# Kernel optimization log

Measured on AMD Instinct MI355X. Metric: run time of the kernel, lower is better.

## Reference

```python
import jax, jax.numpy as jnp
import numpy as np

NUM_HEADS = 8
ATTN_BALANCE = 0.5
EPS = 1e-4  # eps in normalize()


def mp_linear(x, w, gain):
    # MP_Conv with kernel=(1,1): per-output-channel RMS weight renorm then scale.
    # normalize(w): w / (eps + ||w_row|| / sqrt(fan_in)); then * gain / sqrt(fan_in)
    fan_in = w.shape[1]
    n = jnp.linalg.norm(w.astype(jnp.float32), axis=1, keepdims=True)  # (out,1)
    wn = w / (EPS + n / np.sqrt(fan_in))
    wn = wn * (gain / np.sqrt(fan_in))
    return x @ wn.T


def setup_inputs() -> dict:
    key = jax.random.key(0)
    ks = jax.random.split(key, 6)
    B, S, E = 8, 1024, 1024
    H = NUM_HEADS
    return {
        "query": jax.random.normal(ks[0], (B, S, E), jnp.float32),
        "gain_s": jnp.ones((), jnp.float32),
        "gain_t": jnp.ones((), jnp.float32),
        "q_w": jax.random.normal(ks[1], (E, E), jnp.float32),
        "k_w": jax.random.normal(ks[2], (E, E), jnp.float32),
        "v_w": jax.random.normal(ks[3], (E, E), jnp.float32),
        "o_w": jax.random.normal(ks[4], (E, E), jnp.float32),
        "rel_pos_bias": 0.01 * jax.random.normal(ks[5], (H, S, S), jnp.float32),
    }


def reference(query, gain_s, gain_t, q_w, k_w, v_w, o_w, rel_pos_bias):
    # time_dim=0 so the time-dependent branches are inactive; gain_t unused.
    B, S, E = query.shape
    H = NUM_HEADS
    hd = E // H
    # MP projections (1x1 conv == per-position linear), split heads -> (B,H,S,hd)
    q = mp_linear(query, q_w, gain_s).reshape(B, S, H, hd).transpose(0, 2, 1, 3)
    k = mp_linear(query, k_w, gain_s).reshape(B, S, H, hd).transpose(0, 2, 1, 3)
    v = mp_linear(query, v_w, gain_s).reshape(B, S, H, hd).transpose(0, 2, 1, 3)
    # (B,H,S,S) scores, scaled, plus learned relative position bias (seq_len == seq_ln)
    scores = jnp.einsum("bhsd,bhtd->bhst", q, k) / np.sqrt(hd) + rel_pos_bias[None]
    attn = jax.nn.softmax(scores, axis=-1)
    o = jnp.einsum("bhst,bhtd->bhsd", attn, v)
    o = o.transpose(0, 2, 1, 3).reshape(B, S, E)
    out = mp_linear(o, o_w, gain_s)
    # mp_sum residual: lerp(res, out, t) / sqrt((1-t)^2 + t^2)
    t = ATTN_BALANCE
    return (query * (1.0 - t) + out * t) / np.sqrt((1.0 - t) ** 2 + t ** 2)
```

## Files before the change

kernel.cpp:

```cpp
#include <hip/hip_runtime.h>
#include <hip/hip_bf16.h>
#include <math.h>


typedef __attribute__((ext_vector_type(4))) float f32x4;
typedef __attribute__((ext_vector_type(4))) short s16x4;
typedef __attribute__((ext_vector_type(8))) short s16x8;

__device__ __forceinline__ short f2bf(float f) {
  union { __hip_bfloat16 h; short s; } u;
  u.h = __float2bfloat16(f);
  return u.s;
}
__device__ __forceinline__ f32x4 mfma16(s16x8 a, s16x8 b, f32x4 c) {
  return __builtin_amdgcn_mfma_f32_16x16x32_bf16(a, b, c, 0, 0, 0);
}

typedef __attribute__((address_space(1))) const unsigned int* as1_u32p;
typedef __attribute__((address_space(3))) unsigned int* as3_u32p;
__device__ __forceinline__ void g2l16(const short* g, short* l) {
  __builtin_amdgcn_global_load_lds((as1_u32p)g, (as3_u32p)l, 16, 0, 0);
}

__global__ __launch_bounds__(256) void k_wnorm(const float* __restrict__ qw, const float* __restrict__ kw,
                                               const float* __restrict__ vw, const float* __restrict__ ow,
                                               const float* __restrict__ gain, short* __restrict__ wn) {
  const int r = blockIdx.x;
  const int mat = r >> 10;
  const float* W = mat == 0 ? qw : mat == 1 ? kw : mat == 2 ? vw : ow;
  const float* src = W + (size_t)(r & 1023) * 1024;
  const int tid = threadIdx.x;
  f32x4 v = *(const f32x4*)&src[tid * 4];
  float s = v[0]*v[0] + v[1]*v[1] + v[2]*v[2] + v[3]*v[3];
  __shared__ float red[256];
  red[tid] = s; __syncthreads();
  for (int off = 128; off > 0; off >>= 1) {
    if (tid < off) red[tid] += red[tid + off];
    __syncthreads();
  }
  const float scale = gain[0] / (0.0032f + sqrtf(red[0]));
  s16x4 o;
  o[0] = f2bf(v[0]*scale); o[1] = f2bf(v[1]*scale);
  o[2] = f2bf(v[2]*scale); o[3] = f2bf(v[3]*scale);
  *(s16x4*)&wn[(size_t)r * 1024 + tid * 4] = o;
}

__global__ __launch_bounds__(256) void k_cvt(const float* __restrict__ in, short* __restrict__ out, int n4) {
  int idx = blockIdx.x * 256 + threadIdx.x;
  int stride = gridDim.x * 256;
  for (int i = idx; i < n4; i += stride) {
    f32x4 v = ((const f32x4*)in)[i];
    s16x4 o;
    o[0] = f2bf(v[0]); o[1] = f2bf(v[1]); o[2] = f2bf(v[2]); o[3] = f2bf(v[3]);
    ((s16x4*)out)[i] = o;
  }
}

__global__ __launch_bounds__(256) void k_scaleb(const float* __restrict__ in, float* __restrict__ out, int n4) {
  const float L2E = 1.4426950408889634f;
  int idx = blockIdx.x * 256 + threadIdx.x;
  int stride = gridDim.x * 256;
  for (int i = idx; i < n4; i += stride) {
    f32x4 v = ((const f32x4*)in)[i];
    v[0] *= L2E; v[1] *= L2E; v[2] *= L2E; v[3] *= L2E;
    ((f32x4*)out)[i] = v;
  }
}

#define GEMM_K_LOOP(XPTR, WPTR)                                                      \
  const int srw = lane >> 3;                                  \
  const int ssl = lane & 7;                                            \
  const int ql7 = ql & 7;                                                            \
  for (int k0 = 0; k0 < 1024; k0 += 64) {                                            \
    _Pragma("unroll")                                                                \
    for (int i = 0; i < 4; i++) {                                                    \
      const int row = i * 32 + w * 8 + srw;                                          \
      g2l16(&XPTR[(size_t)(m0 + row) * 1024 + k0 + ((ssl ^ srw) << 3)],              \
            &Al[(i * 32 + w * 8) * 64]);                                             \
      g2l16(&WPTR[(size_t)(n0 + row) * 1024 + k0 + ((ssl ^ srw) << 3)],              \
            &Bl[(i * 32 + w * 8) * 64]);                                             \
    }                                                                                \
    __syncthreads();                                                                 \
    _Pragma("unroll")                                                                \
    for (int kc = 0; kc < 2; ++kc) {                                                 \
      s16x8 af[4], bfr[4];                                                           \
      _Pragma("unroll")                                                              \
      for (int i = 0; i < 4; i++) {                                                  \
        const int rA = wm * 64 + i * 16 + ql;                                        \
        af[i] = *(const s16x8*)((const char*)Al + rA * 128 +                         \
                                (((kc * 64 + 16 * hi)) ^ (ql7 << 4)));               \
      }                                                                              \
      _Pragma("unroll")                                                              \
      for (int j = 0; j < 4; j++) {                                                  \
        const int rB = wn_ * 64 + j * 16 + ql;                                       \
        bfr[j] = *(const s16x8*)((const char*)Bl + rB * 128 +                        \
                                 (((kc * 64 + 16 * hi)) ^ (ql7 << 4)));              \
      }                                                                              \
      _Pragma("unroll")                                                              \
      for (int i = 0; i < 4; i++)                                                    \
        _Pragma("unroll")                                                            \
        for (int j = 0; j < 4; j++) acc[i][j] = mfma16(af[i], bfr[j], acc[i][j]);    \
    }                                                                                \
    __syncthreads();                                                                 \
  }

__global__ __launch_bounds__(256) void k_gemm_qkv(const short* __restrict__ X, const short* __restrict__ WN,
                                                  short* __restrict__ Qb, short* __restrict__ Kb,
                                                  short* __restrict__ Vt) {
  __shared__ short Al[128 * 64];
  __shared__ short Bl[128 * 64];
  int f = blockIdx.x + (blockIdx.y << 6) + (blockIdx.z << 9);
  f = (f & 7) * 192 + (f >> 3);
  const int z = f >> 9;
  const short* __restrict__ Wm = WN + (size_t)z * 1048576;
  const int m0 = (f & 63) * 128, n0 = ((f >> 6) & 7) * 128;
  const int tid = threadIdx.x, lane = tid & 63, w = tid >> 6;
  const int hi = lane >> 4, ql = lane & 15;
  const int wm = w >> 1, wn_ = w & 1;
  f32x4 acc[4][4];
#pragma unroll
  for (int i = 0; i < 4; i++)
#pragma unroll
    for (int j = 0; j < 4; j++) acc[i][j] = (f32x4){0.f, 0.f, 0.f, 0.f};
  GEMM_K_LOOP(X, Wm)
  if (z == 2) {
    const int b = m0 >> 10;
    const int sbase = (m0 & 1023) + wm * 64;
#pragma unroll
    for (int i = 0; i < 4; i++) {
#pragma unroll
      for (int j = 0; j < 4; j++) {
        int ng = n0 + wn_ * 64 + j * 16 + ql;
        int h = ng >> 7, d = ng & 127;
        int s = sbase + i * 16 + 4 * hi;
        s16x4 v;
        v[0] = f2bf(acc[i][j][0]); v[1] = f2bf(acc[i][j][1]);
        v[2] = f2bf(acc[i][j][2]); v[3] = f2bf(acc[i][j][3]);
        *(s16x4*)&Vt[(size_t)((b * 8 + h) * 128 + d) * 1024 + s] = v;
      }
    }
  } else {
    short* __restrict__ C = (z == 0) ? Qb : Kb;
#pragma unroll
    for (int i = 0; i < 4; i++) {
      int mg = m0 + wm * 64 + i * 16 + 4 * hi;
#pragma unroll
      for (int j = 0; j < 4; j++) {
        int ng = n0 + wn_ * 64 + j * 16 + ql;
#pragma unroll
        for (int r = 0; r < 4; r++) C[(size_t)(mg + r) * 1024 + ng] = f2bf(acc[i][j][r]);
      }
    }
  }
}

__global__ __launch_bounds__(256) void k_attn(const short* __restrict__ Qb, const short* __restrict__ Kb,
                                              const short* __restrict__ Vt, const float* __restrict__ B2,
                                              short* __restrict__ Ob) {
  __shared__ short lds[64 * 128 + 128 * 64];
  short* Kl = lds;
  short* Vl = lds + 64 * 128;
  int f = blockIdx.x + (blockIdx.y << 4);
  f = (f & 7) * 128 + (f >> 3);
  const int bh = f >> 4, b = bh >> 3, h = bh & 7;
  const int q0 = (f & 15) * 64;
  const int tid = threadIdx.x, w = tid >> 6, lane = tid & 63;
  const int hi = lane >> 4, ql = lane & 15, ql7 = ql & 7;
  const int qrow = q0 + w * 16 + ql;
  const short* __restrict__ qbase = Qb + (size_t)(b * 1024 + qrow) * 1024 + h * 128;
  s16x8 qf[4];
#pragma unroll
  for (int kc = 0; kc < 4; kc++) qf[kc] = *(const s16x8*)&qbase[kc * 32 + 8 * hi];
  float lsum = 0.f;
  f32x4 acc[8];
#pragma unroll
  for (int d = 0; d < 8; d++) acc[d] = (f32x4){0.f, 0.f, 0.f, 0.f};
  const float sc2 = (float)(0.08838834764831845 * 1.4426950408889634);
  const int krow_ = tid >> 4, kslot = tid & 15;
  const int vrow_ = tid >> 3, vslot = tid & 7;
  const short* __restrict__ Kg = Kb + (size_t)(b * 1024) * 1024 + h * 128;
  const short* __restrict__ Vg = Vt + (size_t)bh * 128 * 1024;
  const float* __restrict__ Bg = B2 + (size_t)(h * 1024 + qrow) * 1024;

  s16x8 krA[4], vrA[4], krB[4], vrB[4];
  f32x4 brA[4], brB[4];
#define LOADT(KR, VR, BR, T0)                                                          \
  do {                                                                                 \
    _Pragma("unroll")                                                                  \
    for (int i = 0; i < 4; i++)                                                        \
      KR[i] = *(const s16x8*)&Kg[(size_t)((T0) + i * 16 + krow_) * 1024 + kslot * 8];  \
    _Pragma("unroll")                                                                  \
    for (int i = 0; i < 4; i++)                                                        \
      VR[i] = *(const s16x8*)&Vg[(size_t)(i * 32 + vrow_) * 1024 + (T0) + vslot * 8];  \
    _Pragma("unroll")                                                                  \
    for (int t = 0; t < 4; t++)                                                        \
      BR[t] = *(const f32x4*)&Bg[(T0) + t * 16 + 4 * hi];                              \
  } while (0)

#define STAGE(KR, VR)                                                                  \
  do {                                                                                 \
    _Pragma("unroll")                                                                  \
    for (int i = 0; i < 4; i++) {                                                      \
      int row = i * 16 + krow_;                                                        \
      *(s16x8*)((char*)Kl + row * 256 + ((kslot ^ (row & 7)) << 4)) = KR[i];           \
    }                                                                                  \
    _Pragma("unroll")                                                                  \
    for (int i = 0; i < 4; i++) {                                                      \
      int row = i * 32 + vrow_;                                                        \
      *(s16x8*)((char*)Vl + row * 128 + ((vslot ^ (row & 7)) << 4)) = VR[i];           \
    }                                                                                  \
  } while (0)

#define COMPUTE(BR)                                                                    \
  do {                                                                                 \
    f32x4 st[4];                                                                       \
    __builtin_amdgcn_s_setprio(1);                                                     \
    _Pragma("unroll")                                                                  \
    for (int tb = 0; tb < 4; tb++) {                                                   \
      st[tb] = (f32x4){0.f, 0.f, 0.f, 0.f};                                            \
      _Pragma("unroll")                                                                \
      for (int kc = 0; kc < 4; kc++) {                                                 \
        s16x8 kf = *(const s16x8*)((const char*)Kl + (tb * 16 + ql) * 256 +            \
                                   ((kc * 64 + 16 * hi) ^ (ql7 << 4)));                \
        st[tb] = mfma16(kf, qf[kc], st[tb]);                                           \
      }                                                                                \
    }                                                                                  \
    __builtin_amdgcn_s_setprio(0);                                                     \
    s16x8 pf[2];                                                                       \
    _Pragma("unroll")                                                                  \
    for (int tc = 0; tc < 2; tc++) {                                                   \
      _Pragma("unroll")                                                                \
      for (int r = 0; r < 4; r++) {                                                    \
        float e0 = exp2f(fmaf(st[2 * tc][r],     sc2, BR[2 * tc][r]));                 \
        float e1 = exp2f(fmaf(st[2 * tc + 1][r], sc2, BR[2 * tc + 1][r]));             \
        lsum += e0 + e1;                                                               \
        pf[tc][r] = f2bf(e0);                                                          \
        pf[tc][4 + r] = f2bf(e1);                                                      \
      }                                                                                \
    }                                                                                  \
    __builtin_amdgcn_s_setprio(1);                                                     \
    _Pragma("unroll")                                                                  \
    for (int db = 0; db < 8; db++) {                                                   \
      const char* vbase = (const char*)Vl + (db * 16 + ql) * 128;                      \
      _Pragma("unroll")                                                                \
      for (int tc = 0; tc < 2; tc++) {                                                 \
        s16x4 lo  = *(const s16x4*)(vbase + ((tc * 64 + 8 * hi) ^ (ql7 << 4)));        \
        s16x4 hi4 = *(const s16x4*)(vbase + ((tc * 64 + 32 + 8 * hi) ^ (ql7 << 4)));   \
        s16x8 vf;                                                                      \
        vf[0] = lo[0]; vf[1] = lo[1]; vf[2] = lo[2]; vf[3] = lo[3];                    \
        vf[4] = hi4[0]; vf[5] = hi4[1]; vf[6] = hi4[2]; vf[7] = hi4[3];                 \
        acc[db] = mfma16(vf, pf[tc], acc[db]);                                         \
      }                                                                                \
    }                                                                                  \
    __builtin_amdgcn_s_setprio(0);                                                     \
  } while (0)

  LOADT(krA, vrA, brA, 0);
  for (int ih = 0; ih < 8; ++ih) {
    const int t0 = ih * 128;
    __syncthreads();
    STAGE(krA, vrA);
    LOADT(krB, vrB, brB, t0 + 64);
    __syncthreads();
    COMPUTE(brA);
    __syncthreads();
    STAGE(krB, vrB);
    if (ih < 7) LOADT(krA, vrA, brA, t0 + 128);
    __syncthreads();
    COMPUTE(brB);
  }
  lsum += __shfl_xor(lsum, 16);
  lsum += __shfl_xor(lsum, 32);
  const float invl = 1.f / lsum;
  __syncthreads();
  short* Ol = lds;
#pragma unroll
  for (int db = 0; db < 8; db++) {
    s16x4 v;
    v[0] = f2bf(acc[db][0] * invl); v[1] = f2bf(acc[db][1] * invl);
    v[2] = f2bf(acc[db][2] * invl); v[3] = f2bf(acc[db][3] * invl);
    *(s16x4*)&Ol[(w * 16 + ql) * 136 + db * 16 + 4 * hi] = v;
  }
  __syncthreads();
#pragma unroll
  for (int it = 0; it < 4; ++it) {
    int idx = tid + it * 256;
    int row = idx >> 4, c = idx & 15;
    *(s16x8*)&Ob[(size_t)(b * 1024 + q0 + row) * 1024 + h * 128 + c * 8] = *(const s16x8*)&Ol[row * 136 + c * 8];
  }
#undef LOADT
#undef STAGE
#undef COMPUTE
}

__global__ __launch_bounds__(256) void k_gemm_o(const short* __restrict__ X, const short* __restrict__ Wm,
                                                const float* __restrict__ Qin, float* __restrict__ Out) {
  __shared__ short Al[128 * 64];
  __shared__ short Bl[128 * 64];
  int f = blockIdx.x + (blockIdx.y << 6);
  f = (f & 7) * 64 + (f >> 3);
  const int m0 = (f & 63) * 128, n0 = (f >> 6) * 128;
  const int tid = threadIdx.x, lane = tid & 63, w = tid >> 6;
  const int hi = lane >> 4, ql = lane & 15;
  const int wm = w >> 1, wn_ = w & 1;
  f32x4 acc[4][4];
#pragma unroll
  for (int i = 0; i < 4; i++)
#pragma unroll
    for (int j = 0; j < 4; j++) acc[i][j] = (f32x4){0.f, 0.f, 0.f, 0.f};
  GEMM_K_LOOP(X, Wm)
#pragma unroll
  for (int i = 0; i < 4; i++) {
    int mg = m0 + wm * 64 + i * 16 + 4 * hi;
#pragma unroll
    for (int j = 0; j < 4; j++) {
      int ng = n0 + wn_ * 64 + j * 16 + ql;
#pragma unroll
      for (int r = 0; r < 4; r++) {
        size_t idx = (size_t)(mg + r) * 1024 + ng;
        Out[idx] = (Qin[idx] + acc[i][j][r]) * 0.7071067811865476f;
      }
    }
  }
}

extern "C" void kernel_launch(void* const* d_in, const int* in_sizes, int n_in,
                              void* d_out, int out_size, void* d_ws, size_t ws_size,
                              hipStream_t stream) {
  (void)in_sizes; (void)n_in; (void)out_size; (void)ws_size;
  const float* query = (const float*)d_in[0];
  const float* gain_s = (const float*)d_in[1];
  const float* qw = (const float*)d_in[3];
  const float* kw = (const float*)d_in[4];
  const float* vw = (const float*)d_in[5];
  const float* ow = (const float*)d_in[6];
  const float* bias = (const float*)d_in[7];
  float* out = (float*)d_out;

  short* ws = (short*)d_ws;
  short* s_wn = ws;
  short* s_x  = s_wn + 4 * 1048576;
  short* s_Q  = s_x + 8388608;
  short* s_K  = s_Q + 8388608;
  short* s_Vt = s_K + 8388608;
  float* s_B2 = (float*)(s_Vt + 8388608);
  short* s_O  = s_x;

  k_wnorm<<<dim3(4096), dim3(256), 0, stream>>>(qw, kw, vw, ow, gain_s, s_wn);
  k_cvt<<<dim3(2048), dim3(256), 0, stream>>>(query, s_x, 2097152);
  k_scaleb<<<dim3(2048), dim3(256), 0, stream>>>(bias, s_B2, 2097152);
  k_gemm_qkv<<<dim3(64, 8, 3), dim3(256), 0, stream>>>(s_x, s_wn, s_Q, s_K, s_Vt);
  k_attn<<<dim3(16, 64), dim3(256), 0, stream>>>(s_Q, s_K, s_Vt, s_B2, s_O);
  k_gemm_o<<<dim3(64, 8), dim3(256), 0, stream>>>(s_O, s_wn + 3 * 1048576, query, out);
}
```

Before: 326.8 us.

## Double-buffer GEMM LDS, stage GEMM epilogue stores, store bias as bf16

The GEMM k-loop now double-buffers its LDS tiles, prefetching the next K tile while the current one is computed, and uses explicit waitcnt and barrier calls plus setprio around the MFMA block. The QKV and O GEMMs drop the XCD-aware block remapping. The QKV epilogue now stages results through LDS so global stores are coalesced 16-byte writes, including the transposed V. The relative position bias is pre-scaled into bf16 rather than fp32, halving its traffic in attention, and the attention loop swaps __syncthreads for finer-grained waitcnt and barrier calls. Together these aim to cut memory stalls and bandwidth, but bf16 bias loses precision and doubled LDS may lower occupancy.

```diff
diff --git a/kernel.cpp b/kernel.cpp
--- a/kernel.cpp
+++ b/kernel.cpp
@@ -12,6 +12,11 @@
   u.h = __float2bfloat16(f);
   return u.s;
 }
+__device__ __forceinline__ float bf2f(short s) {
+  union { short s; __hip_bfloat16 h; } u;
+  u.s = s;
+  return __bfloat162float(u.h);
+}
 __device__ __forceinline__ f32x4 mfma16(s16x8 a, s16x8 b, f32x4 c) {
   return __builtin_amdgcn_mfma_f32_16x16x32_bf16(a, b, c, 0, 0, 0);
 }
@@ -21,6 +26,11 @@
 __device__ __forceinline__ void g2l16(const short* g, short* l) {
   __builtin_amdgcn_global_load_lds((as1_u32p)g, (as3_u32p)l, 16, 0, 0);
 }
+
+#define ASM_VMCNT0 asm volatile("s_waitcnt vmcnt(0)" ::: "memory")
+#define ASM_LGKM0  asm volatile("s_waitcnt lgkmcnt(0)" ::: "memory")
+#define SFENCE     __builtin_amdgcn_sched_barrier(0)
+#define BARRIER    __builtin_amdgcn_s_barrier()
 
 __global__ __launch_bounds__(256) void k_wnorm(const float* __restrict__ qw, const float* __restrict__ kw,
                                                const float* __restrict__ vw, const float* __restrict__ ow,
@@ -56,14 +66,16 @@
   }
 }
 
-__global__ __launch_bounds__(256) void k_scaleb(const float* __restrict__ in, float* __restrict__ out, int n4) {
+__global__ __launch_bounds__(256) void k_scaleb(const float* __restrict__ in, short* __restrict__ out, int n4) {
   const float L2E = 1.4426950408889634f;
   int idx = blockIdx.x * 256 + threadIdx.x;
   int stride = gridDim.x * 256;
   for (int i = idx; i < n4; i += stride) {
     f32x4 v = ((const f32x4*)in)[i];
-    v[0] *= L2E; v[1] *= L2E; v[2] *= L2E; v[3] *= L2E;
-    ((f32x4*)out)[i] = v;
+    s16x4 o;
+    o[0] = f2bf(v[0]*L2E); o[1] = f2bf(v[1]*L2E);
+    o[2] = f2bf(v[2]*L2E); o[3] = f2bf(v[3]*L2E);
+    ((s16x4*)out)[i] = o;
   }
 }
 
@@ -71,49 +83,66 @@
   const int srw = lane >> 3;                                  \
   const int ssl = lane & 7;                                            \
   const int ql7 = ql & 7;                                                            \
-  for (int k0 = 0; k0 < 1024; k0 += 64) {                                            \
+  {                                                                                  \
     _Pragma("unroll")                                                                \
     for (int i = 0; i < 4; i++) {                                                    \
       const int row = i * 32 + w * 8 + srw;                                          \
-      g2l16(&XPTR[(size_t)(m0 + row) * 1024 + k0 + ((ssl ^ srw) << 3)],              \
-            &Al[(i * 32 + w * 8) * 64]);                                             \
-      g2l16(&WPTR[(size_t)(n0 + row) * 1024 + k0 + ((ssl ^ srw) << 3)],              \
-            &Bl[(i * 32 + w * 8) * 64]);                                             \
+      g2l16(&XPTR[(size_t)(m0 + row) * 1024 + ((ssl ^ srw) << 3)],                   \
+            &Al[0][(i * 32 + w * 8) * 64]);                                          \
+      g2l16(&WPTR[(size_t)(n0 + row) * 1024 + ((ssl ^ srw) << 3)],                   \
+            &Bl[0][(i * 32 + w * 8) * 64]);                                          \
     }                                                                                \
-    __syncthreads();                                                                 \
-    _Pragma("unroll")                                                                \
-    for (int kc = 0; kc < 2; ++kc) {                                                 \
-      s16x8 af[4], bfr[4];                                                           \
+    ASM_VMCNT0; SFENCE; BARRIER; SFENCE;                                             \
+    int bi = 0;                                                                      \
+    for (int t = 0; t < 16; ++t) {                                                   \
+      if (t < 15) {                                                                  \
+        const int k1 = (t + 1) * 64;                                                 \
+        _Pragma("unroll")                                                            \
+        for (int i = 0; i < 4; i++) {                                                \
+          const int row = i * 32 + w * 8 + srw;                                      \
+          g2l16(&XPTR[(size_t)(m0 + row) * 1024 + k1 + ((ssl ^ srw) << 3)],          \
+                &Al[bi ^ 1][(i * 32 + w * 8) * 64]);                                 \
+          g2l16(&WPTR[(size_t)(n0 + row) * 1024 + k1 + ((ssl ^ srw) << 3)],          \
+                &Bl[bi ^ 1][(i * 32 + w * 8) * 64]);                                 \
+        }                                                                            \
+      }                                                                              \
+      const char* alp = (const char*)&Al[bi][0];                                     \
+      const char* blp = (const char*)&Bl[bi][0];                                     \
+      __builtin_amdgcn_s_setprio(1);                                                 \
       _Pragma("unroll")                                                              \
-      for (int i = 0; i < 4; i++) {                                                  \
-        const int rA = wm * 64 + i * 16 + ql;                                        \
-        af[i] = *(const s16x8*)((const char*)Al + rA * 128 +                         \
-                                (((kc * 64 + 16 * hi)) ^ (ql7 << 4)));               \
+      for (int kc = 0; kc < 2; ++kc) {                                               \
+        s16x8 af[4], bfr[4];                                                         \
+        _Pragma("unroll")                                                            \
+        for (int i = 0; i < 4; i++) {                                                \
+          const int rA = wm * 64 + i * 16 + ql;                                      \
+          af[i] = *(const s16x8*)(alp + rA * 128 +                                   \
+                                  ((kc * 64 + 16 * hi) ^ (ql7 << 4)));               \
+        }                                                                            \
+        _Pragma("unroll")                                                            \
+        for (int j = 0; j < 4; j++) {                                                \
+          const int rB = wn_ * 64 + j * 16 + ql;                                     \
+          bfr[j] = *(const s16x8*)(blp + rB * 128 +                                  \
+                                   ((kc * 64 + 16 * hi) ^ (ql7 << 4)));              \
+        }                                                                            \
+        _Pragma("unroll")                                                            \
+        for (int i = 0; i < 4; i++)                                                  \
+          _Pragma("unroll")                                                          \
+          for (int j = 0; j < 4; j++) acc[i][j] = mfma16(af[i], bfr[j], acc[i][j]);  \
       }                                                                              \
-      _Pragma("unroll")                                                              \
-      for (int j = 0; j < 4; j++) {                                                  \
-        const int rB = wn_ * 64 + j * 16 + ql;                                       \
-        bfr[j] = *(const s16x8*)((const char*)Bl + rB * 128 +                        \
-                                 (((kc * 64 + 16 * hi)) ^ (ql7 << 4)));              \
-      }                                                                              \
-      _Pragma("unroll")                                                              \
-      for (int i = 0; i < 4; i++)                                                    \
-        _Pragma("unroll")                                                            \
-        for (int j = 0; j < 4; j++) acc[i][j] = mfma16(af[i], bfr[j], acc[i][j]);    \
+      __builtin_amdgcn_s_setprio(0);                                                 \
+      ASM_VMCNT0; SFENCE; BARRIER; SFENCE;                                           \
+      bi ^= 1;                                                                       \
     }                                                                                \
-    __syncthreads();                                                                 \
   }
 
 __global__ __launch_bounds__(256) void k_gemm_qkv(const short* __restrict__ X, const short* __restrict__ WN,
                                                   short* __restrict__ Qb, short* __restrict__ Kb,
                                                   short* __restrict__ Vt) {
-  __shared__ short Al[128 * 64];
-  __shared__ short Bl[128 * 64];
-  int f = blockIdx.x + (blockIdx.y << 6) + (blockIdx.z << 9);
-  f = (f & 7) * 192 + (f >> 3);
-  const int z = f >> 9;
+  __shared__ short Al[2][128 * 64];
+  __shared__ short Bl[2][128 * 64];
+  const int z = blockIdx.z;
   const short* __restrict__ Wm = WN + (size_t)z * 1048576;
-  const int m0 = (f & 63) * 128, n0 = ((f >> 6) & 7) * 128;
+  const int m0 = blockIdx.x * 128, n0 = blockIdx.y * 128;
   const int tid = threadIdx.x, lane = tid & 63, w = tid >> 6;
   const int hi = lane >> 4, ql = lane & 15;
   const int wm = w >> 1, wn_ = w & 1;
@@ -123,39 +152,52 @@
 #pragma unroll
     for (int j = 0; j < 4; j++) acc[i][j] = (f32x4){0.f, 0.f, 0.f, 0.f};
   GEMM_K_LOOP(X, Wm)
+  short* Cl = &Al[0][0];
   if (z == 2) {
-    const int b = m0 >> 10;
-    const int sbase = (m0 & 1023) + wm * 64;
 #pragma unroll
     for (int i = 0; i < 4; i++) {
 #pragma unroll
       for (int j = 0; j < 4; j++) {
-        int ng = n0 + wn_ * 64 + j * 16 + ql;
-        int h = ng >> 7, d = ng & 127;
-        int s = sbase + i * 16 + 4 * hi;
-        s16x4 v;
-        v[0] = f2bf(acc[i][j][0]); v[1] = f2bf(acc[i][j][1]);
-        v[2] = f2bf(acc[i][j][2]); v[3] = f2bf(acc[i][j][3]);
-        *(s16x4*)&Vt[(size_t)((b * 8 + h) * 128 + d) * 1024 + s] = v;
+        int col = wn_ * 64 + j * 16 + ql;
+        int rowb = wm * 64 + i * 16 + 4 * hi;
+#pragma unroll
+        for (int r = 0; r < 4; r++) Cl[col * 128 + rowb + r] = f2bf(acc[i][j][r]);
       }
+    }
+    __syncthreads();
+    const int b = m0 >> 10, sb = (m0 & 1023);
+#pragma unroll
+    for (int it = 0; it < 8; ++it) {
+      int idx = tid + it * 256;
+      int dl = idx >> 4, c = idx & 15;
+      int ng = n0 + dl, h = ng >> 7, d = ng & 127;
+      *(s16x8*)&Vt[(size_t)((b * 8 + h) * 128 + d) * 1024 + sb + c * 8] =
+          *(const s16x8*)&Cl[dl * 128 + c * 8];
     }
   } else {
     short* __restrict__ C = (z == 0) ? Qb : Kb;
 #pragma unroll
     for (int i = 0; i < 4; i++) {
-      int mg = m0 + wm * 64 + i * 16 + 4 * hi;
 #pragma unroll
       for (int j = 0; j < 4; j++) {
-        int ng = n0 + wn_ * 64 + j * 16 + ql;
-#pragma unroll
-        for (int r = 0; r < 4; r++) C[(size_t)(mg + r) * 1024 + ng] = f2bf(acc[i][j][r]);
+        int col = wn_ * 64 + j * 16 + ql;
+        int rowb = wm * 64 + i * 16 + 4 * hi;
+#pragma unroll
+        for (int r = 0; r < 4; r++) Cl[(rowb + r) * 128 + col] = f2bf(acc[i][j][r]);
       }
     }
+    __syncthreads();
+#pragma unroll
+    for (int it = 0; it < 8; ++it) {
+      int idx = tid + it * 256;
+      int row = idx >> 4, c = idx & 15;
+      *(s16x8*)&C[(size_t)(m0 + row) * 1024 + n0 + c * 8] = *(const s16x8*)&Cl[row * 128 + c * 8];
+    }
   }
 }
 
 __global__ __launch_bounds__(256) void k_attn(const short* __restrict__ Qb, const short* __restrict__ Kb,
-                                              const short* __restrict__ Vt, const float* __restrict__ B2,
+                                              const short* __restrict__ Vt, const short* __restrict__ B2,
                                               short* __restrict__ Ob) {
   __shared__ short lds[64 * 128 + 128 * 64];
   short* Kl = lds;
@@ -180,10 +222,10 @@
   const int vrow_ = tid >> 3, vslot = tid & 7;
   const short* __restrict__ Kg = Kb + (size_t)(b * 1024) * 1024 + h * 128;
   const short* __restrict__ Vg = Vt + (size_t)bh * 128 * 1024;
-  const float* __restrict__ Bg = B2 + (size_t)(h * 1024 + qrow) * 1024;
+  const short* __restrict__ Bg = B2 + (size_t)(h * 1024 + qrow) * 1024;
 
   s16x8 krA[4], vrA[4], krB[4], vrB[4];
-  f32x4 brA[4], brB[4];
+  s16x4 brA[4], brB[4];
 #define LOADT(KR, VR, BR, T0)                                                          \
   do {                                                                                 \
     _Pragma("unroll")                                                                  \
@@ -194,7 +236,7 @@
       VR[i] = *(const s16x8*)&Vg[(size_t)(i * 32 + vrow_) * 1024 + (T0) + vslot * 8];  \
     _Pragma("unroll")                                                                  \
     for (int t = 0; t < 4; t++)                                                        \
-      BR[t] = *(const f32x4*)&Bg[(T0) + t * 16 + 4 * hi];                              \
+      BR[t] = *(const s16x4*)&Bg[(T0) + t * 16 + 4 * hi];                              \
   } while (0)
 
 #define STAGE(KR, VR)                                                                  \
@@ -231,8 +273,8 @@
     for (int tc = 0; tc < 2; tc++) {                                                   \
       _Pragma("unroll")                                                                \
       for (int r = 0; r < 4; r++) {                                                    \
-        float e0 = exp2f(fmaf(st[2 * tc][r],     sc2, BR[2 * tc][r]));                 \
-        float e1 = exp2f(fmaf(st[2 * tc + 1][r], sc2, BR[2 * tc + 1][r]));             \
+        float e0 = exp2f(fmaf(st[2 * tc][r],     sc2, bf2f(BR[2 * tc][r])));           \
+        float e1 = exp2f(fmaf(st[2 * tc + 1][r], sc2, bf2f(BR[2 * tc + 1][r])));       \
         lsum += e0 + e1;                                                               \
         pf[tc][r] = f2bf(e0);                                                          \
         pf[tc][4 + r] = f2bf(e1);                                                      \
@@ -258,21 +300,22 @@
   LOADT(krA, vrA, brA, 0);
   for (int ih = 0; ih < 8; ++ih) {
     const int t0 = ih * 128;
-    __syncthreads();
+    ASM_VMCNT0; SFENCE;
     STAGE(krA, vrA);
     LOADT(krB, vrB, brB, t0 + 64);
-    __syncthreads();
+    ASM_LGKM0; SFENCE; BARRIER; SFENCE;
     COMPUTE(brA);
-    __syncthreads();
+    BARRIER; SFENCE;
+    ASM_VMCNT0; SFENCE;
     STAGE(krB, vrB);
     if (ih < 7) LOADT(krA, vrA, brA, t0 + 128);
-    __syncthreads();
+    ASM_LGKM0; SFENCE; BARRIER; SFENCE;
     COMPUTE(brB);
+    BARRIER; SFENCE;
   }
   lsum += __shfl_xor(lsum, 16);
   lsum += __shfl_xor(lsum, 32);
   const float invl = 1.f / lsum;
-  __syncthreads();
   short* Ol = lds;
 #pragma unroll
   for (int db = 0; db < 8; db++) {
@@ -295,11 +338,9 @@
 
 __global__ __launch_bounds__(256) void k_gemm_o(const short* __restrict__ X, const short* __restrict__ Wm,
                                                 const float* __restrict__ Qin, float* __restrict__ Out) {
-  __shared__ short Al[128 * 64];
-  __shared__ short Bl[128 * 64];
-  int f = blockIdx.x + (blockIdx.y << 6);
-  f = (f & 7) * 64 + (f >> 3);
-  const int m0 = (f & 63) * 128, n0 = (f >> 6) * 128;
+  __shared__ short Al[2][128 * 64];
+  __shared__ short Bl[2][128 * 64];
+  const int m0 = blockIdx.x * 128, n0 = blockIdx.y * 128;
   const int tid = threadIdx.x, lane = tid & 63, w = tid >> 6;
   const int hi = lane >> 4, ql = lane & 15;
   const int wm = w >> 1, wn_ = w & 1;
@@ -340,10 +381,10 @@
   short* ws = (short*)d_ws;
   short* s_wn = ws;
   short* s_x  = s_wn + 4 * 1048576;
-  short* s_Q  = s_x + 8388608;
+  short* s_B2 = s_x + 8388608;
+  short* s_Q  = s_B2 + 8388608;
   short* s_K  = s_Q + 8388608;
   short* s_Vt = s_K + 8388608;
-  float* s_B2 = (float*)(s_Vt + 8388608);
   short* s_O  = s_x;
 
   k_wnorm<<<dim3(4096), dim3(256), 0, stream>>>(qw, kw, vw, ow, gain_s, s_wn);
```

Result: faster. 307.9 us (-5.8%).
